# Performance work log

Hardware: AMD Instinct MI355X
Metric: run time of the kernel (lower is better)

Reference implementation:

```python
import jax, jax.numpy as jnp
import numpy as np

N_NODES = 50000
N_EDGES = 800000
D_IN = 64
D_OUT = 64

def setup_inputs() -> dict:
    key = jax.random.key(0)
    k1, k2, k3, k4 = jax.random.split(key, 4)
    x = jax.random.normal(k1, (N_NODES, D_IN), dtype=jnp.float32)
    # Linear(in, out, bias=False): weight shape [out, in], Kaiming-uniform-ish scale
    bound = 1.0 / np.sqrt(D_IN)
    W = jax.random.uniform(k2, (D_OUT, D_IN), dtype=jnp.float32, minval=-bound, maxval=bound)
    src = jax.random.randint(k3, (N_EDGES,), 0, N_NODES, dtype=jnp.int32)
    dst = jax.random.randint(k4, (N_EDGES,), 0, N_NODES, dtype=jnp.int32)
    return {"x": x, "W": W, "src": src, "dst": dst}

def reference(x, W, src, dst):
    # update_all(copy_src, sum): for each edge (s, d), add x[s] into node d
    agg = jax.ops.segment_sum(x[src], dst, num_segments=N_NODES)  # [N, D_IN]
    # linear1 (bias=False); dropout is identity at inference
    h = jnp.einsum('nd,od->no', agg, W)  # [N, D_OUT]
    h = jax.nn.relu(h)
    # is_normalize=False -> skip L2 normalize; residual adds input node features
    return h + x
```

## Files before the change

### kernel.cpp

```cpp
#include <hip/hip_runtime.h>

#define D 64
#define NCHUNK 64
#define NOCT 8
#define CAP 48
#define HIST_BLOCKS (NCHUNK * NOCT)
#define GEMM_BLOCKS 2048

__device__ __forceinline__ float bflo(unsigned u) { return __uint_as_float(u << 16); }
__device__ __forceinline__ float bfhi(unsigned u) { return __uint_as_float(u & 0xffff0000u); }
__device__ __forceinline__ unsigned short f2bf(float f) {
    unsigned b = __float_as_uint(f);
    return (unsigned short)((b + 0x7fffu + ((b >> 16) & 1u)) >> 16);
}

__global__ __launch_bounds__(256) void hist_gemm_kernel(
    const float* __restrict__ x, const float* __restrict__ W,
    const int* __restrict__ dst, int* __restrict__ blockhist, int* __restrict__ rank,
    unsigned short* __restrict__ ybf, int n_nodes, int ne) {
    __shared__ int lds[6272];
    if (blockIdx.x < HIST_BLOCKS) {
        const int chunk = blockIdx.x >> 3;
        const int oct = blockIdx.x & (NOCT - 1);
        const int csz = (ne + NCHUNK - 1) / NCHUNK;
        const int e0 = chunk * csz, e1 = min(e0 + csz, ne);
        const int octn = (n_nodes + NOCT - 1) / NOCT;
        const int dlo = oct * octn, dhi = min(dlo + octn, n_nodes);
        for (int i = threadIdx.x; i < dhi - dlo; i += 256) lds[i] = 0;
        __syncthreads();
        for (int e = e0 + threadIdx.x; e < e1; e += 256) {
            const int d = dst[e];
            if (d >= dlo && d < dhi) rank[e] = atomicAdd(&lds[d - dlo], 1);
        }
        __syncthreads();
        int* bh = blockhist + (size_t)chunk * n_nodes;
        for (int i = threadIdx.x; i < dhi - dlo; i += 256) bh[dlo + i] = lds[i];
    } else {
        float* As = (float*)lds;
        const int tid = threadIdx.x;
        const int w = tid >> 6, o = tid & 63;
        const float4* W4 = (const float4*)W;
        float4 wr[16];
#pragma unroll
        for (int k = 0; k < 16; ++k) wr[k] = W4[o * 16 + k];
        const int ngrp = (n_nodes + 3) >> 2;
        for (int grp = blockIdx.x - HIST_BLOCKS; grp < ngrp; grp += GEMM_BLOCKS) {
            const int base = grp * 4;
            __syncthreads();
            if (base * D + tid < n_nodes * D) As[tid] = x[base * D + tid];
            __syncthreads();
            const int n = base + w;
            if (n < n_nodes) {
                float h = 0.f;
#pragma unroll
                for (int k = 0; k < 16; ++k) {
                    const float4 a = *(const float4*)&As[w * D + k * 4];
                    h = fmaf(a.x, wr[k].x, h);
                    h = fmaf(a.y, wr[k].y, h);
                    h = fmaf(a.z, wr[k].z, h);
                    h = fmaf(a.w, wr[k].w, h);
                }
                ybf[(size_t)n * D + o] = f2bf(h);
            }
        }
    }
}

__global__ void colscan_kernel(int* __restrict__ blockhist, int* __restrict__ counts,
                               int n_nodes) {
    const int d = blockIdx.x * 256 + threadIdx.x;
    if (d >= n_nodes) return;
    int acc = 0;
    for (int c0 = 0; c0 < NCHUNK; c0 += 8) {
        int h[8];
#pragma unroll
        for (int k = 0; k < 8; ++k) h[k] = blockhist[(size_t)(c0 + k) * n_nodes + d];
#pragma unroll
        for (int k = 0; k < 8; ++k) {
            blockhist[(size_t)(c0 + k) * n_nodes + d] = acc;
            acc += h[k];
        }
    }
    counts[d] = acc;
}

__global__ void place_kernel(const int* __restrict__ src, const int* __restrict__ dst,
                             const int* __restrict__ blockhist, const int* __restrict__ rank,
                             int* __restrict__ esrc, int n_nodes, int ne, int csz) {
    const int e = blockIdx.x * 256 + threadIdx.x;
    if (e >= ne) return;
    const int d = dst[e];
    const int chunk = e / csz;
    const int slot = blockhist[(size_t)chunk * n_nodes + d] + rank[e];
    if (slot < CAP) esrc[d * CAP + slot] = src[e];
}

__global__ void gather_kernel(const int* __restrict__ counts, const int* __restrict__ esrc,
                              const unsigned short* __restrict__ ybf,
                              const float* __restrict__ x, float* __restrict__ out,
                              int n_nodes) {
    const int tid = threadIdx.x;
    const int w = tid >> 6, lane = tid & 63;
    const int g = lane >> 3, m = lane & 7;
    const uint4* Y4 = (const uint4*)ybf;
    const float4* x4 = (const float4*)x;
    float4* out4 = (float4*)out;
    const int waveId = blockIdx.x * 4 + w;
    const int nWaves = gridDim.x * 4;

    for (int n = waveId; n < n_nodes; n += nWaves) {
        int c = counts[n];
        if (c > CAP) c = CAP;
        const int base = n * CAP;
        float acc[8] = {0.f, 0.f, 0.f, 0.f, 0.f, 0.f, 0.f, 0.f};
        for (int j = 0; j < c; j += 8) {
            const int e = j + g;
            const int s = esrc[base + (e < c ? e : c - 1)];
            const uint4 v = Y4[(size_t)s * 8 + m];
            if (e < c) {
                acc[0] += bflo(v.x); acc[1] += bfhi(v.x);
                acc[2] += bflo(v.y); acc[3] += bfhi(v.y);
                acc[4] += bflo(v.z); acc[5] += bfhi(v.z);
                acc[6] += bflo(v.w); acc[7] += bfhi(v.w);
            }
        }
#pragma unroll
        for (int k = 0; k < 8; ++k) {
            acc[k] += __shfl_xor(acc[k], 8);
            acc[k] += __shfl_xor(acc[k], 16);
            acc[k] += __shfl_xor(acc[k], 32);
        }
        if (lane < 8) {
            const float4 xa = x4[(size_t)n * 16 + lane * 2];
            const float4 xb = x4[(size_t)n * 16 + lane * 2 + 1];
            float4 oa, ob;
            oa.x = fmaxf(acc[0], 0.f) + xa.x;
            oa.y = fmaxf(acc[1], 0.f) + xa.y;
            oa.z = fmaxf(acc[2], 0.f) + xa.z;
            oa.w = fmaxf(acc[3], 0.f) + xa.w;
            ob.x = fmaxf(acc[4], 0.f) + xb.x;
            ob.y = fmaxf(acc[5], 0.f) + xb.y;
            ob.z = fmaxf(acc[6], 0.f) + xb.z;
            ob.w = fmaxf(acc[7], 0.f) + xb.w;
            out4[(size_t)n * 16 + lane * 2] = oa;
            out4[(size_t)n * 16 + lane * 2 + 1] = ob;
        }
    }
}

extern "C" void kernel_launch(void* const* d_in, const int* in_sizes, int n_in,
                              void* d_out, int out_size, void* d_ws, size_t ws_size,
                              hipStream_t stream) {
    const float* x = (const float*)d_in[0];
    const float* W = (const float*)d_in[1];
    const int* src = (const int*)d_in[2];
    const int* dst = (const int*)d_in[3];
    float* out = (float*)d_out;

    const int n_nodes = in_sizes[0] / D;
    const int n_edges = in_sizes[2];
    const int csz = (n_edges + NCHUNK - 1) / NCHUNK;

    int* blockhist = (int*)d_ws;
    int* rank      = blockhist + (size_t)NCHUNK * n_nodes;
    int* counts    = rank + n_edges;
    int* esrc      = counts + n_nodes;
    unsigned short* ybf = (unsigned short*)(esrc + (size_t)n_nodes * CAP);

    const int ngrid = (n_nodes + 255) / 256;
    const int egrid = (n_edges + 255) / 256;

    hist_gemm_kernel<<<HIST_BLOCKS + GEMM_BLOCKS, 256, 0, stream>>>(
        x, W, dst, blockhist, rank, ybf, n_nodes, n_edges);
    colscan_kernel<<<ngrid, 256, 0, stream>>>(blockhist, counts, n_nodes);
    place_kernel<<<egrid, 256, 0, stream>>>(src, dst, blockhist, rank, esrc,
                                            n_nodes, n_edges, csz);
    gather_kernel<<<2048, 256, 0, stream>>>(counts, esrc, ybf, x, out, n_nodes);
}
```

Baseline: 154.0 us.

## Split bf16 projection into column halves and gather each half separately

The projected features are stored as two separate 32-column bf16 arrays, and the gather runs twice, once per half. This shrinks the working set of each gather pass so it fits better in cache. The histogram and rank arrays are narrowed from int to 16-bit, which cuts their memory traffic. The GEMM now processes 16 nodes per block iteration with float4 loads. The cost is reading esrc and counts twice plus one extra kernel launch, and the 16-bit counters assume fewer than 65536 edges per destination.

```diff
diff --git a/kernel.cpp b/kernel.cpp
--- a/kernel.cpp
+++ b/kernel.cpp
@@ -16,9 +16,11 @@
 
 __global__ __launch_bounds__(256) void hist_gemm_kernel(
     const float* __restrict__ x, const float* __restrict__ W,
-    const int* __restrict__ dst, int* __restrict__ blockhist, int* __restrict__ rank,
-    unsigned short* __restrict__ ybf, int n_nodes, int ne) {
+    const int* __restrict__ dst, unsigned short* __restrict__ blockhist,
+    unsigned short* __restrict__ rank, unsigned short* __restrict__ yA,
+    unsigned short* __restrict__ yB, int n_nodes, int ne) {
     __shared__ int lds[6272];
+    const int tid = threadIdx.x;
     if (blockIdx.x < HIST_BLOCKS) {
         const int chunk = blockIdx.x >> 3;
         const int oct = blockIdx.x & (NOCT - 1);
@@ -26,48 +28,56 @@
         const int e0 = chunk * csz, e1 = min(e0 + csz, ne);
         const int octn = (n_nodes + NOCT - 1) / NOCT;
         const int dlo = oct * octn, dhi = min(dlo + octn, n_nodes);
-        for (int i = threadIdx.x; i < dhi - dlo; i += 256) lds[i] = 0;
+        for (int i = tid; i < dhi - dlo; i += 256) lds[i] = 0;
         __syncthreads();
-        for (int e = e0 + threadIdx.x; e < e1; e += 256) {
+        for (int e = e0 + tid; e < e1; e += 256) {
             const int d = dst[e];
-            if (d >= dlo && d < dhi) rank[e] = atomicAdd(&lds[d - dlo], 1);
+            if (d >= dlo && d < dhi)
+                rank[e] = (unsigned short)atomicAdd(&lds[d - dlo], 1);
         }
         __syncthreads();
-        int* bh = blockhist + (size_t)chunk * n_nodes;
-        for (int i = threadIdx.x; i < dhi - dlo; i += 256) bh[dlo + i] = lds[i];
+        unsigned short* bh = blockhist + (size_t)chunk * n_nodes;
+        for (int i = tid; i < dhi - dlo; i += 256) bh[dlo + i] = (unsigned short)lds[i];
     } else {
         float* As = (float*)lds;
-        const int tid = threadIdx.x;
         const int w = tid >> 6, o = tid & 63;
         const float4* W4 = (const float4*)W;
         float4 wr[16];
 #pragma unroll
         for (int k = 0; k < 16; ++k) wr[k] = W4[o * 16 + k];
-        const int ngrp = (n_nodes + 3) >> 2;
+        const float4* x4 = (const float4*)x;
+        const int ngrp = (n_nodes + 15) >> 4;
         for (int grp = blockIdx.x - HIST_BLOCKS; grp < ngrp; grp += GEMM_BLOCKS) {
-            const int base = grp * 4;
+            const int base = grp * 16;
             __syncthreads();
-            if (base * D + tid < n_nodes * D) As[tid] = x[base * D + tid];
+            const int idx = base * 16 + tid;
+            if (idx < n_nodes * 16) ((float4*)As)[tid] = x4[idx];
             __syncthreads();
-            const int n = base + w;
-            if (n < n_nodes) {
-                float h = 0.f;
 #pragma unroll
-                for (int k = 0; k < 16; ++k) {
-                    const float4 a = *(const float4*)&As[w * D + k * 4];
-                    h = fmaf(a.x, wr[k].x, h);
-                    h = fmaf(a.y, wr[k].y, h);
-                    h = fmaf(a.z, wr[k].z, h);
-                    h = fmaf(a.w, wr[k].w, h);
+            for (int i = 0; i < 4; ++i) {
+                const int n = base + w * 4 + i;
+                if (n < n_nodes) {
+                    const float* a = &As[(w * 4 + i) * D];
+                    float h = 0.f;
+#pragma unroll
+                    for (int k = 0; k < 16; ++k) {
+                        const float4 av = *(const float4*)&a[k * 4];
+                        h = fmaf(av.x, wr[k].x, h);
+                        h = fmaf(av.y, wr[k].y, h);
+                        h = fmaf(av.z, wr[k].z, h);
+                        h = fmaf(av.w, wr[k].w, h);
+                    }
+                    const unsigned short hb = f2bf(h);
+                    if (o < 32) yA[n * 32 + o] = hb;
+                    else        yB[n * 32 + (o & 31)] = hb;
                 }
-                ybf[(size_t)n * D + o] = f2bf(h);
             }
         }
     }
 }
 
-__global__ void colscan_kernel(int* __restrict__ blockhist, int* __restrict__ counts,
-                               int n_nodes) {
+__global__ void colscan_kernel(unsigned short* __restrict__ blockhist,
+                               int* __restrict__ counts, int n_nodes) {
     const int d = blockIdx.x * 256 + threadIdx.x;
     if (d >= n_nodes) return;
     int acc = 0;
@@ -77,7 +87,7 @@
         for (int k = 0; k < 8; ++k) h[k] = blockhist[(size_t)(c0 + k) * n_nodes + d];
 #pragma unroll
         for (int k = 0; k < 8; ++k) {
-            blockhist[(size_t)(c0 + k) * n_nodes + d] = acc;
+            blockhist[(size_t)(c0 + k) * n_nodes + d] = (unsigned short)acc;
             acc += h[k];
         }
     }
@@ -85,24 +95,26 @@
 }
 
 __global__ void place_kernel(const int* __restrict__ src, const int* __restrict__ dst,
-                             const int* __restrict__ blockhist, const int* __restrict__ rank,
+                             const unsigned short* __restrict__ blockhist,
+                             const unsigned short* __restrict__ rank,
                              int* __restrict__ esrc, int n_nodes, int ne, int csz) {
     const int e = blockIdx.x * 256 + threadIdx.x;
     if (e >= ne) return;
     const int d = dst[e];
     const int chunk = e / csz;
-    const int slot = blockhist[(size_t)chunk * n_nodes + d] + rank[e];
+    const int slot = (int)blockhist[(size_t)chunk * n_nodes + d] + (int)rank[e];
     if (slot < CAP) esrc[d * CAP + slot] = src[e];
 }
 
-__global__ void gather_kernel(const int* __restrict__ counts, const int* __restrict__ esrc,
-                              const unsigned short* __restrict__ ybf,
-                              const float* __restrict__ x, float* __restrict__ out,
-                              int n_nodes) {
+__global__ void gather_half_kernel(const int* __restrict__ counts,
+                                   const int* __restrict__ esrc,
+                                   const unsigned short* __restrict__ yh,
+                                   const float* __restrict__ x, float* __restrict__ out,
+                                   int n_nodes, int fo0) {
     const int tid = threadIdx.x;
     const int w = tid >> 6, lane = tid & 63;
-    const int g = lane >> 3, m = lane & 7;
-    const uint4* Y4 = (const uint4*)ybf;
+    const int g = lane >> 2, m = lane & 3;
+    const uint4* Y4 = (const uint4*)yh;
     const float4* x4 = (const float4*)x;
     float4* out4 = (float4*)out;
     const int waveId = blockIdx.x * 4 + w;
@@ -113,11 +125,11 @@
         if (c > CAP) c = CAP;
         const int base = n * CAP;
         float acc[8] = {0.f, 0.f, 0.f, 0.f, 0.f, 0.f, 0.f, 0.f};
-        for (int j = 0; j < c; j += 8) {
+        for (int j = 0; j < c; j += 16) {
             const int e = j + g;
-            const int s = esrc[base + (e < c ? e : c - 1)];
-            const uint4 v = Y4[(size_t)s * 8 + m];
             if (e < c) {
+                const int s = esrc[base + e];
+                const uint4 v = Y4[(size_t)s * 4 + m];
                 acc[0] += bflo(v.x); acc[1] += bfhi(v.x);
                 acc[2] += bflo(v.y); acc[3] += bfhi(v.y);
                 acc[4] += bflo(v.z); acc[5] += bfhi(v.z);
@@ -126,13 +138,15 @@
         }
 #pragma unroll
         for (int k = 0; k < 8; ++k) {
+            acc[k] += __shfl_xor(acc[k], 4);
             acc[k] += __shfl_xor(acc[k], 8);
             acc[k] += __shfl_xor(acc[k], 16);
             acc[k] += __shfl_xor(acc[k], 32);
         }
-        if (lane < 8) {
-            const float4 xa = x4[(size_t)n * 16 + lane * 2];
-            const float4 xb = x4[(size_t)n * 16 + lane * 2 + 1];
+        if (lane < 4) {
+            const int fo = n * 16 + fo0 + lane * 2;
+            const float4 xa = x4[fo];
+            const float4 xb = x4[fo + 1];
             float4 oa, ob;
             oa.x = fmaxf(acc[0], 0.f) + xa.x;
             oa.y = fmaxf(acc[1], 0.f) + xa.y;
@@ -142,8 +156,8 @@
             ob.y = fmaxf(acc[5], 0.f) + xb.y;
             ob.z = fmaxf(acc[6], 0.f) + xb.z;
             ob.w = fmaxf(acc[7], 0.f) + xb.w;
-            out4[(size_t)n * 16 + lane * 2] = oa;
-            out4[(size_t)n * 16 + lane * 2 + 1] = ob;
+            out4[fo] = oa;
+            out4[fo + 1] = ob;
         }
     }
 }
@@ -161,19 +175,21 @@
     const int n_edges = in_sizes[2];
     const int csz = (n_edges + NCHUNK - 1) / NCHUNK;
 
-    int* blockhist = (int*)d_ws;
-    int* rank      = blockhist + (size_t)NCHUNK * n_nodes;
-    int* counts    = rank + n_edges;
-    int* esrc      = counts + n_nodes;
-    unsigned short* ybf = (unsigned short*)(esrc + (size_t)n_nodes * CAP);
+    unsigned short* blockhist = (unsigned short*)d_ws;
+    unsigned short* rank = blockhist + (size_t)NCHUNK * n_nodes;
+    int* counts = (int*)(rank + n_edges + (n_edges & 1));
+    int* esrc = counts + n_nodes;
+    unsigned short* yA = (unsigned short*)(esrc + (size_t)n_nodes * CAP);
+    unsigned short* yB = yA + (size_t)n_nodes * 32;
 
     const int ngrid = (n_nodes + 255) / 256;
     const int egrid = (n_edges + 255) / 256;
 
     hist_gemm_kernel<<<HIST_BLOCKS + GEMM_BLOCKS, 256, 0, stream>>>(
-        x, W, dst, blockhist, rank, ybf, n_nodes, n_edges);
+        x, W, dst, blockhist, rank, yA, yB, n_nodes, n_edges);
     colscan_kernel<<<ngrid, 256, 0, stream>>>(blockhist, counts, n_nodes);
     place_kernel<<<egrid, 256, 0, stream>>>(src, dst, blockhist, rank, esrc,
                                             n_nodes, n_edges, csz);
-    gather_kernel<<<2048, 256, 0, stream>>>(counts, esrc, ybf, x, out, n_nodes);
+    gather_half_kernel<<<2048, 256, 0, stream>>>(counts, esrc, yA, x, out, n_nodes, 0);
+    gather_half_kernel<<<2048, 256, 0, stream>>>(counts, esrc, yB, x, out, n_nodes, 8);
 }
```

Result: slower. 175.4 us (+13.9%).

## Pack histograms into 16-bit LDS counters and recompute ranks in place kernel

Applied to the files above, without the earlier changes.

The histogram stage now keeps per-chunk node counts as packed 16-bit counters in shared memory, so one block covers half the node range instead of an eighth. The place kernel reloads the scanned offsets into LDS and uses atomics there to assign slots, which removes the global rank array and its write and read traffic. The GEMM is split into its own kernel with W transposed into LDS and 16 nodes per block iteration. The costs are more LDS atomic work inside place, a larger shared-memory footprint per block, and serialisation of the GEMM and histogram launches that used to share one kernel.

```diff
diff --git a/kernel.cpp b/kernel.cpp
--- a/kernel.cpp
+++ b/kernel.cpp
@@ -1,11 +1,9 @@
 #include <hip/hip_runtime.h>
 
 #define D 64
-#define NCHUNK 64
-#define NOCT 8
+#define NCHUNK 128
+#define NHALF 2
 #define CAP 48
-#define HIST_BLOCKS (NCHUNK * NOCT)
-#define GEMM_BLOCKS 2048
 
 __device__ __forceinline__ float bflo(unsigned u) { return __uint_as_float(u << 16); }
 __device__ __forceinline__ float bfhi(unsigned u) { return __uint_as_float(u & 0xffff0000u); }
@@ -14,60 +12,79 @@
     return (unsigned short)((b + 0x7fffu + ((b >> 16) & 1u)) >> 16);
 }
 
-__global__ __launch_bounds__(256) void hist_gemm_kernel(
+__global__ __launch_bounds__(256) void gemm_kernel(
     const float* __restrict__ x, const float* __restrict__ W,
-    const int* __restrict__ dst, int* __restrict__ blockhist, int* __restrict__ rank,
-    unsigned short* __restrict__ ybf, int n_nodes, int ne) {
-    __shared__ int lds[6272];
-    if (blockIdx.x < HIST_BLOCKS) {
-        const int chunk = blockIdx.x >> 3;
-        const int oct = blockIdx.x & (NOCT - 1);
-        const int csz = (ne + NCHUNK - 1) / NCHUNK;
-        const int e0 = chunk * csz, e1 = min(e0 + csz, ne);
-        const int octn = (n_nodes + NOCT - 1) / NOCT;
-        const int dlo = oct * octn, dhi = min(dlo + octn, n_nodes);
-        for (int i = threadIdx.x; i < dhi - dlo; i += 256) lds[i] = 0;
+    unsigned short* __restrict__ y, int n_nodes) {
+    __shared__ float Wt[64 * 65];
+    __shared__ float As[16 * 64];
+    const int tid = threadIdx.x;
+    for (int i = tid; i < 4096; i += 256) {
+        const int o = i >> 6, k = i & 63;
+        Wt[k * 65 + o] = W[i];
+    }
+    const int w = tid >> 6, o = tid & 63;
+    const float4* x4 = (const float4*)x;
+    const int ngrp = (n_nodes + 15) >> 4;
+    for (int grp = blockIdx.x; grp < ngrp; grp += gridDim.x) {
+        const int base = grp * 16;
         __syncthreads();
-        for (int e = e0 + threadIdx.x; e < e1; e += 256) {
-            const int d = dst[e];
-            if (d >= dlo && d < dhi) rank[e] = atomicAdd(&lds[d - dlo], 1);
-        }
+        const int idx = base * 16 + tid;
+        if (idx < n_nodes * 16) ((float4*)As)[tid] = x4[idx];
         __syncthreads();
-        int* bh = blockhist + (size_t)chunk * n_nodes;
-        for (int i = threadIdx.x; i < dhi - dlo; i += 256) bh[dlo + i] = lds[i];
-    } else {
-        float* As = (float*)lds;
-        const int tid = threadIdx.x;
-        const int w = tid >> 6, o = tid & 63;
-        const float4* W4 = (const float4*)W;
-        float4 wr[16];
-#pragma unroll
-        for (int k = 0; k < 16; ++k) wr[k] = W4[o * 16 + k];
-        const int ngrp = (n_nodes + 3) >> 2;
-        for (int grp = blockIdx.x - HIST_BLOCKS; grp < ngrp; grp += GEMM_BLOCKS) {
-            const int base = grp * 4;
-            __syncthreads();
-            if (base * D + tid < n_nodes * D) As[tid] = x[base * D + tid];
-            __syncthreads();
-            const int n = base + w;
-            if (n < n_nodes) {
-                float h = 0.f;
-#pragma unroll
-                for (int k = 0; k < 16; ++k) {
-                    const float4 a = *(const float4*)&As[w * D + k * 4];
-                    h = fmaf(a.x, wr[k].x, h);
-                    h = fmaf(a.y, wr[k].y, h);
-                    h = fmaf(a.z, wr[k].z, h);
-                    h = fmaf(a.w, wr[k].w, h);
-                }
-                ybf[(size_t)n * D + o] = f2bf(h);
-            }
-        }
-    }
-}
-
-__global__ void colscan_kernel(int* __restrict__ blockhist, int* __restrict__ counts,
-                               int n_nodes) {
+        const float* a0 = &As[(w * 4 + 0) * 64];
+        const float* a1 = &As[(w * 4 + 1) * 64];
+        const float* a2 = &As[(w * 4 + 2) * 64];
+        const float* a3 = &As[(w * 4 + 3) * 64];
+        float h0 = 0.f, h1 = 0.f, h2 = 0.f, h3 = 0.f;
+#pragma unroll
+        for (int k = 0; k < 64; ++k) {
+            const float wv = Wt[k * 65 + o];
+            h0 = fmaf(a0[k], wv, h0);
+            h1 = fmaf(a1[k], wv, h1);
+            h2 = fmaf(a2[k], wv, h2);
+            h3 = fmaf(a3[k], wv, h3);
+        }
+        const int n0 = base + w * 4;
+        if (n0 + 3 < n_nodes) {
+            y[(size_t)(n0 + 0) * D + o] = f2bf(h0);
+            y[(size_t)(n0 + 1) * D + o] = f2bf(h1);
+            y[(size_t)(n0 + 2) * D + o] = f2bf(h2);
+            y[(size_t)(n0 + 3) * D + o] = f2bf(h3);
+        } else {
+            if (n0 + 0 < n_nodes) y[(size_t)(n0 + 0) * D + o] = f2bf(h0);
+            if (n0 + 1 < n_nodes) y[(size_t)(n0 + 1) * D + o] = f2bf(h1);
+            if (n0 + 2 < n_nodes) y[(size_t)(n0 + 2) * D + o] = f2bf(h2);
+            if (n0 + 3 < n_nodes) y[(size_t)(n0 + 3) * D + o] = f2bf(h3);
+        }
+    }
+}
+
+__global__ __launch_bounds__(256) void hist_kernel(
+    const int* __restrict__ dst, unsigned short* __restrict__ blockhist,
+    int n_nodes, int ne) {
+    __shared__ unsigned int lw[12544];
+    const int c = blockIdx.x >> 1, h = blockIdx.x & 1;
+    const int csz = (ne + NCHUNK - 1) / NCHUNK;
+    const int e0 = c * csz, e1 = min(e0 + csz, ne);
+    const int hn = (n_nodes + NHALF - 1) / NHALF;
+    const int dlo = h * hn, dhi = min(dlo + hn, n_nodes);
+    const int nw = (dhi - dlo + 1) >> 1;
+    for (int i = threadIdx.x; i < nw; i += 256) lw[i] = 0;
+    __syncthreads();
+    for (int e = e0 + threadIdx.x; e < e1; e += 256) {
+        const int d = dst[e];
+        if (d >= dlo && d < dhi) {
+            const int r = d - dlo;
+            atomicAdd(&lw[r >> 1], 1u << ((r & 1) * 16));
+        }
+    }
+    __syncthreads();
+    unsigned int* bh = (unsigned int*)(blockhist + (size_t)c * n_nodes + dlo);
+    for (int i = threadIdx.x; i < nw; i += 256) bh[i] = lw[i];
+}
+
+__global__ void colscan_kernel(unsigned short* __restrict__ blockhist,
+                               int* __restrict__ counts, int n_nodes) {
     const int d = blockIdx.x * 256 + threadIdx.x;
     if (d >= n_nodes) return;
     int acc = 0;
@@ -77,22 +94,36 @@
         for (int k = 0; k < 8; ++k) h[k] = blockhist[(size_t)(c0 + k) * n_nodes + d];
 #pragma unroll
         for (int k = 0; k < 8; ++k) {
-            blockhist[(size_t)(c0 + k) * n_nodes + d] = acc;
+            blockhist[(size_t)(c0 + k) * n_nodes + d] = (unsigned short)acc;
             acc += h[k];
         }
     }
     counts[d] = acc;
 }
 
-__global__ void place_kernel(const int* __restrict__ src, const int* __restrict__ dst,
-                             const int* __restrict__ blockhist, const int* __restrict__ rank,
-                             int* __restrict__ esrc, int n_nodes, int ne, int csz) {
-    const int e = blockIdx.x * 256 + threadIdx.x;
-    if (e >= ne) return;
-    const int d = dst[e];
-    const int chunk = e / csz;
-    const int slot = blockhist[(size_t)chunk * n_nodes + d] + rank[e];
-    if (slot < CAP) esrc[d * CAP + slot] = src[e];
+__global__ __launch_bounds__(256) void place_kernel(
+    const int* __restrict__ src, const int* __restrict__ dst,
+    const unsigned short* __restrict__ blockhist, int* __restrict__ esrc,
+    int n_nodes, int ne) {
+    __shared__ unsigned int lw[12544];
+    const int c = blockIdx.x >> 1, h = blockIdx.x & 1;
+    const int csz = (ne + NCHUNK - 1) / NCHUNK;
+    const int e0 = c * csz, e1 = min(e0 + csz, ne);
+    const int hn = (n_nodes + NHALF - 1) / NHALF;
+    const int dlo = h * hn, dhi = min(dlo + hn, n_nodes);
+    const int nw = (dhi - dlo + 1) >> 1;
+    const unsigned int* bh = (const unsigned int*)(blockhist + (size_t)c * n_nodes + dlo);
+    for (int i = threadIdx.x; i < nw; i += 256) lw[i] = bh[i];
+    __syncthreads();
+    for (int e = e0 + threadIdx.x; e < e1; e += 256) {
+        const int d = dst[e];
+        if (d >= dlo && d < dhi) {
+            const int r = d - dlo;
+            const unsigned old = atomicAdd(&lw[r >> 1], 1u << ((r & 1) * 16));
+            const int slot = (old >> ((r & 1) * 16)) & 0xffff;
+            if (slot < CAP) esrc[d * CAP + slot] = src[e];
+        }
+    }
 }
 
 __global__ void gather_kernel(const int* __restrict__ counts, const int* __restrict__ esrc,
@@ -159,21 +190,18 @@
 
     const int n_nodes = in_sizes[0] / D;
     const int n_edges = in_sizes[2];
-    const int csz = (n_edges + NCHUNK - 1) / NCHUNK;
-
-    int* blockhist = (int*)d_ws;
-    int* rank      = blockhist + (size_t)NCHUNK * n_nodes;
-    int* counts    = rank + n_edges;
-    int* esrc      = counts + n_nodes;
+
+    unsigned short* blockhist = (unsigned short*)d_ws;
+    int* counts = (int*)(blockhist + (size_t)NCHUNK * n_nodes);
+    int* esrc = counts + n_nodes;
     unsigned short* ybf = (unsigned short*)(esrc + (size_t)n_nodes * CAP);
 
     const int ngrid = (n_nodes + 255) / 256;
-    const int egrid = (n_edges + 255) / 256;
-
-    hist_gemm_kernel<<<HIST_BLOCKS + GEMM_BLOCKS, 256, 0, stream>>>(
-        x, W, dst, blockhist, rank, ybf, n_nodes, n_edges);
+
+    gemm_kernel<<<1024, 256, 0, stream>>>(x, W, ybf, n_nodes);
+    hist_kernel<<<NCHUNK * NHALF, 256, 0, stream>>>(dst, blockhist, n_nodes, n_edges);
     colscan_kernel<<<ngrid, 256, 0, stream>>>(blockhist, counts, n_nodes);
-    place_kernel<<<egrid, 256, 0, stream>>>(src, dst, blockhist, rank, esrc,
-                                            n_nodes, n_edges, csz);
+    place_kernel<<<NCHUNK * NHALF, 256, 0, stream>>>(src, dst, blockhist, esrc,
+                                                     n_nodes, n_edges);
     gather_kernel<<<2048, 256, 0, stream>>>(counts, esrc, ybf, x, out, n_nodes);
 }
```

Result: no change. 153.6 us (-0.3%).
